# Kernel tuning notes

Hardware: AMD Instinct MI355X
Metric: run time of the kernel (lower is better)

Reference implementation:

```python
import jax, jax.numpy as jnp
import numpy as np

B, CIN, COUT, H, W = 4, 128, 128, 128, 128
K = 3
K2 = K * K
PAD = 1
EPS = 1e-5


def setup_inputs() -> dict:
    key = jax.random.key(0)
    ks = jax.random.split(key, 11)
    def n(k, shp, s=0.05):
        return jax.random.normal(k, shp, jnp.float32) * s
    return {
        'x': jax.random.normal(ks[0], (B, CIN, H, W), jnp.float32),
        'w_attn': n(ks[1], (COUT, CIN, 3, 3)), 'b_attn': n(ks[2], (COUT,)),
        'w_feat': n(ks[3], (COUT, CIN, 3, 3)), 'b_feat': n(ks[4], (COUT,)),
        'w_org': n(ks[5], (COUT, COUT, 3, 3)), 'b_org': n(ks[6], (COUT,)),
        'w_off': n(ks[7], (2 * K2, COUT, 3, 3), 0.01), 'b_off': n(ks[8], (2 * K2,), 0.01),
        'w_mask': n(ks[9], (K2, COUT, 3, 3)), 'b_mask': n(ks[10], (K2,)),
    }


def _conv(x, w, b, stride=1, pad=1):
    y = jax.lax.conv_general_dilated(
        x, w, (stride, stride), [(pad, pad), (pad, pad)],
        dimension_numbers=('NCHW', 'OIHW', 'NCHW'))
    return y + b[None, :, None, None]


def _instance_norm(x):
    mu = jnp.mean(x, axis=(2, 3), keepdims=True)
    var = jnp.var(x, axis=(2, 3), keepdims=True)
    return (x - mu) * jax.lax.rsqrt(var + EPS)


def _lrelu(x):
    return jnp.where(x > 0, x, 0.2 * x)


def _bilinear_gather(img, y, x):
    Hin, Win = img.shape[2], img.shape[3]
    y0 = jnp.floor(y)
    x0 = jnp.floor(x)
    wy = y - y0
    wx = x - x0
    y0i = y0.astype(jnp.int32)
    x0i = x0.astype(jnp.int32)
    acc = None
    for dy, dx, w in ((0, 0, (1 - wy) * (1 - wx)), (0, 1, (1 - wy) * wx),
                      (1, 0, wy * (1 - wx)), (1, 1, wy * wx)):
        yi = y0i + dy
        xi = x0i + dx
        valid = (yi >= 0) & (yi < Hin) & (xi >= 0) & (xi < Win)
        yc = jnp.clip(yi, 0, Hin - 1)
        xc = jnp.clip(xi, 0, Win - 1)
        g = jax.vmap(lambda im, yy, xx: im[:, yy, xx])(img, yc, xc)  # [B,C,K2,H,W]
        ww = (w * valid.astype(img.dtype))[:, None]
        acc = g * ww if acc is None else acc + g * ww
    return acc


def _deform_conv(x, w_org, b_org, w_off, b_off, w_mask, b_mask):
    # torchvision-style modulated deform_conv2d, K=3, stride=1, pad=1
    b, c, h, w = x.shape
    offset = _conv(x, w_off, b_off, 1, 1)                       # [B,2*K2,H,W]
    mask = jax.nn.sigmoid(_conv(x, w_mask, b_mask, 1, 1))       # [B,K2,H,W]
    off = offset.reshape(b, K2, 2, h, w)
    dy, dx = off[:, :, 0], off[:, :, 1]
    ki = jnp.arange(K2, dtype=jnp.float32) // K                 # tap row (row-major)
    kj = jnp.arange(K2, dtype=jnp.float32) % K                  # tap col
    hh = jnp.arange(h, dtype=jnp.float32)
    wwg = jnp.arange(w, dtype=jnp.float32)
    y = dy + hh[None, None, :, None] + ki[None, :, None, None] - PAD
    xs = dx + wwg[None, None, None, :] + kj[None, :, None, None] - PAD
    samp = _bilinear_gather(x, y, xs)                           # [B,C,K2,H,W]
    samp = samp * mask[:, None]
    wflat = w_org.reshape(w_org.shape[0], c, K2)
    out = jnp.einsum('bckhw,ock->bohw', samp, wflat)
    return out + b_org[None, :, None, None]


def reference(x, w_attn, b_attn, w_feat, b_feat, w_org, b_org,
              w_off, b_off, w_mask, b_mask):
    attn = jax.nn.sigmoid(_conv(x, w_attn, b_attn, 1, 1))
    x_feat = _lrelu(_instance_norm(_conv(x, w_feat, b_feat, 1, 1)))
    x_attned = x_feat * attn
    dconv = _deform_conv(x_attned, w_org, b_org, w_off, b_off, w_mask, b_mask)
    x_valid = _lrelu(_instance_norm(dconv))
    return x_attned + x_valid * (1 - attn)
```

## Files before the change

### kernel.cpp

```cpp
#include <hip/hip_runtime.h>
#include <math.h>

#define BDIM 256
constexpr int BB = 4, Cc = 128, Hh = 128, Wd = 128, HW = Hh * Wd;
constexpr float EPSv = 1e-5f;

typedef __attribute__((ext_vector_type(8))) short short8v;
typedef __attribute__((ext_vector_type(4))) float floatx4;
typedef __attribute__((ext_vector_type(2))) float float2v;

#define MFMA16(a, b, c) __builtin_amdgcn_mfma_f32_16x16x32_bf16((a), (b), (c), 0, 0, 0)

__device__ __forceinline__ float sigmoidf_(float v) { return 1.f / (1.f + __expf(-v)); }

__device__ __forceinline__ unsigned short f2bf(float f) {
    union { float f; unsigned u; } v; v.f = f;
    unsigned r = v.u + 0x7FFFu + ((v.u >> 16) & 1u);
    return (unsigned short)(r >> 16);
}
__device__ __forceinline__ unsigned cvtpk(float a, float b) {
    unsigned r;
    asm("v_cvt_pk_bf16_f32 %0, %1, %2" : "=v"(r) : "v"(a), "v"(b));
    return r;
}
__device__ __forceinline__ float bflo(unsigned u) { union { unsigned u; float f; } v; v.u = u << 16; return v.f; }
__device__ __forceinline__ float bfhi(unsigned u) { union { unsigned u; float f; } v; v.u = u & 0xFFFF0000u; return v.f; }
__device__ __forceinline__ float bfu(unsigned short u) { union { unsigned u; float f; } v; v.u = ((unsigned)u) << 16; return v.f; }
__device__ __forceinline__ float2v unpk2(unsigned u) {
    union { unsigned x[2]; float2v f; } v;
    v.x[0] = u << 16;
    v.x[1] = u & 0xFFFF0000u;
    return v.f;
}

__device__ __forceinline__ void barrier_lgkm() {
    asm volatile("s_waitcnt lgkmcnt(0)" ::: "memory");
    __builtin_amdgcn_s_barrier();
}

__device__ __forceinline__ void gload16(const void* g, void* l) {
    __builtin_amdgcn_global_load_lds(
        (const __attribute__((address_space(1))) unsigned int*)g,
        (__attribute__((address_space(3))) unsigned int*)l, 16, 0, 0);
}

__global__ void repack_all_k(const float* __restrict__ w_attn, const float* __restrict__ w_feat,
                             const float* __restrict__ w_org, const float* __restrict__ w_off,
                             const float* __restrict__ w_mask, const float* __restrict__ b_off,
                             const float* __restrict__ b_mask,
                             unsigned short* __restrict__ wpkAF, unsigned short* __restrict__ wpkO,
                             unsigned short* __restrict__ wpkOM, float* __restrict__ bom) {
    int idx = blockIdx.x * BDIM + threadIdx.x;
    const int TOT = 26 * 18432;
    if (idx < TOT) {
        int seg = idx / 18432, rem = idx % 18432;
        int i = rem & 7, lane = (rem >> 3) & 63, tap = (rem >> 9) % 9, chunk = rem / (9 * 512);
        int lco = lane & 15;
        int ci = chunk * 32 + (lane >> 4) * 8 + i;
        float v = 0.f;
        unsigned short* dst;
        int didx;
        if (seg < 16) {
            int cot = seg & 7;
            const float* w = (seg < 8) ? w_attn : w_feat;
            int co = cot * 16 + lco;
            v = w[((size_t)co * Cc + ci) * 9 + tap];
            dst = wpkAF; didx = idx;
        } else if (seg < 24) {
            int co = (seg - 16) * 16 + lco;
            v = w_org[((size_t)co * Cc + ci) * 9 + tap];
            dst = wpkO; didx = idx - 16 * 18432;
        } else {
            int co = (seg - 24) * 16 + lco;
            if (co < 18)      v = w_off[((size_t)co * Cc + ci) * 9 + tap];
            else if (co < 27) v = w_mask[((size_t)(co - 18) * Cc + ci) * 9 + tap];
            dst = wpkOM; didx = idx - 24 * 18432;
        }
        dst[didx] = f2bf(v);
    } else if (idx < TOT + 32) {
        int j = idx - TOT;
        bom[j] = (j < 18) ? b_off[j] : (j < 27 ? b_mask[j - 18] : 0.f);
    }
}

__global__ __launch_bounds__(256) void tobf_k(const float* __restrict__ x,
                                              unsigned short* __restrict__ dst) {
    const int h = blockIdx.x, b = blockIdx.y;
    const int t = threadIdx.x;
    __shared__ unsigned short lt[16][128];
    const int ciq = t >> 4, wg = t & 15;
    const int w = t >> 1, half = t & 1;
    for (int s = 0; s < 8; s++) {
        const float* p = x + ((size_t)(b * 128 + s * 16 + ciq) * HW + h * 128 + wg * 8);
        float4 a = *(const float4*)p;
        float4 c = *(const float4*)(p + 4);
        *(uint4*)&lt[ciq][wg * 8] =
            make_uint4(cvtpk(a.x, a.y), cvtpk(a.z, a.w), cvtpk(c.x, c.y), cvtpk(c.z, c.w));
        __syncthreads();
        unsigned r[4];
#pragma unroll
        for (int k = 0; k < 4; k++) {
            unsigned lo = lt[half * 8 + 2 * k][w];
            unsigned hi = lt[half * 8 + 2 * k + 1][w];
            r[k] = lo | (hi << 16);
        }
        *(uint4*)(dst + ((size_t)b * HW + h * 128 + w) * 128 + s * 16 + half * 8) =
            make_uint4(r[0], r[1], r[2], r[3]);
        __syncthreads();
    }
}

template <int COTPB, int WCO, bool SWZ>
__global__ __launch_bounds__(256, 2) void conv3_k(
    const unsigned short* __restrict__ src, const unsigned short* __restrict__ wpk,
    const float* __restrict__ biasA, const float* __restrict__ biasB,
    int bsplit, int sigsplit,
    float* __restrict__ out, int ldc, int ch0) {
    constexpr int ROWS = 2;
    constexpr int WPX = 4 / WCO;
    constexpr int PXW = 128 / WPX;
    constexpr int PS = PXW / 16;
    constexpr int HB = 128 / ROWS;

    const int t = threadIdx.x;
    const int lane = t & 63, llo = t & 15, lhi = (t >> 4) & 3;
    const int widu = __builtin_amdgcn_readfirstlane(t >> 6);
    const int wr = widu / WPX, wc = widu % WPX;

    int cbi, h0, b;
    if (SWZ) {
        int n = blockIdx.x;
        int xcd = n & 7, j = n >> 3;
        int g = (j >> 2) * 8 + xcd;
        cbi = j & 3;
        h0 = (g % HB) * ROWS;
        b = g / HB;
    } else {
        cbi = 0;
        h0 = ((int)blockIdx.x % HB) * ROWS;
        b = (int)blockIdx.x / HB;
    }
    const int cotbase = cbi * COTPB + wr * 2;

    __shared__ unsigned short xs[2][4][4][128][8];

    floatx4 acc[2][ROWS][PS];
#pragma unroll
    for (int c = 0; c < 2; c++)
#pragma unroll
        for (int row = 0; row < ROWS; row++)
#pragma unroll
            for (int ps = 0; ps < PS; ps++) acc[c][row][ps] = (floatx4){0.f, 0.f, 0.f, 0.f};

    const unsigned short* srcb = src + ((size_t)b * HW + (size_t)(h0 - 1) * 128) * 128;

    auto stage = [&](int chunk, int buf) {
        const unsigned short* sb = srcb + chunk * 32 + widu * 8;
        unsigned short* db = &xs[buf][widu][0][0][0];
#pragma unroll
        for (int i = 0; i < 8; i++) {
            const unsigned short* g = sb + (size_t)(i * 64 + lane) * 128;
            gload16(g, db + i * 512);
        }
    };

    short8v afr[9][2];

    stage(0, 0);
    __syncthreads();

    for (int chunk = 0; chunk < 4; ++chunk) {
        const int buf = chunk & 1;
        if (chunk < 3) stage(chunk + 1, buf ^ 1);
#pragma unroll
        for (int tap = 0; tap < 9; tap++)
#pragma unroll
            for (int c = 0; c < 2; c++)
                afr[tap][c] = *(const short8v*)(wpk +
                    ((((size_t)(cotbase + c) * 4 + chunk) * 9 + tap) * 64 + lane) * 8);
        const int wcb = wc * PXW;
#pragma unroll
        for (int tap = 0; tap < 9; ++tap) {
            const int r = tap / 3, dx = tap % 3;
#pragma unroll
            for (int row = 0; row < ROWS; row++) {
                const int rowr = row + r;
                const int hh = h0 - 1 + rowr;
                if ((unsigned)hh < 128u) {
#pragma unroll
                    for (int ps = 0; ps < PS; ps++) {
                        int colr = wcb + ps * 16 + llo + dx - 1;
                        int colc = min(max(colr, 0), 127);
                        short8v bfv = *(const short8v*)&xs[buf][lhi][rowr][colc][0];
                        if (colr != colc) bfv = (short8v)(short)0;
#pragma unroll
                        for (int c = 0; c < 2; c++)
                            acc[c][row][ps] = MFMA16(afr[tap][c], bfv, acc[c][row][ps]);
                    }
                }
            }
        }
        __syncthreads();
    }

    const int cbase = cbi * (COTPB * 16);
    const float* bp = (cbase < bsplit) ? biasA : biasB;
    const int bshift = (cbase < bsplit) ? 0 : bsplit;
    const bool dosig = cbase < sigsplit;
#pragma unroll
    for (int c = 0; c < 2; c++)
#pragma unroll
        for (int row = 0; row < ROWS; row++)
#pragma unroll
            for (int ps = 0; ps < PS; ps++)
#pragma unroll
                for (int reg = 0; reg < 4; reg++) {
                    int co = cbase + (wr * 2 + c) * 16 + lhi * 4 + reg;
                    int px = wc * PXW + ps * 16 + llo;
                    float v = acc[c][row][ps][reg] + bp[co - bshift];
                    if (dosig) v = sigmoidf_(v);
                    out[((size_t)b * ldc + ch0 + co) * HW + (h0 + row) * Wd + px] = v;
                }
}

__global__ __launch_bounds__(256) void inorm_stats_k(const float* __restrict__ src,
                                                     float* __restrict__ mu, float* __restrict__ rsig,
                                                     int chTot, int ch0) {
    const int bc = blockIdx.x;
    const int b = bc >> 7, c = bc & 127;
    const float4* p = (const float4*)(src + ((size_t)b * chTot + ch0 + c) * HW);
    float s = 0.f, s2 = 0.f;
    for (int i = threadIdx.x; i < HW / 4; i += BDIM) {
        float4 v = p[i];
        s += v.x + v.y + v.z + v.w;
        s2 += v.x * v.x + v.y * v.y + v.z * v.z + v.w * v.w;
    }
    __shared__ float ss[BDIM], sq[BDIM];
    int t = threadIdx.x;
    ss[t] = s; sq[t] = s2;
    __syncthreads();
    for (int off = BDIM / 2; off > 0; off >>= 1) {
        if (t < off) { ss[t] += ss[t + off]; sq[t] += sq[t + off]; }
        __syncthreads();
    }
    if (t == 0) {
        float m = ss[0] / HW;
        float var = sq[0] / HW - m * m;
        mu[bc] = m;
        rsig[bc] = rsqrtf(var + EPSv);
    }
}

__global__ __launch_bounds__(256) void xattned2_k(const float* __restrict__ rawAF,
                                                  const float* __restrict__ mu,
                                                  const float* __restrict__ rsig,
                                                  unsigned short* __restrict__ xabfG) {
    const int seg = blockIdx.x, h = blockIdx.y, b = blockIdx.z;
    const int t = threadIdx.x;
    __shared__ unsigned short la[64][128];
    const int px4 = t & 15, cl = t >> 4;
#pragma unroll
    for (int p = 0; p < 8; p++) {
        int c = p * 16 + cl;
        int plane = b * 128 + c;
        size_t pixo = (size_t)h * Wd + seg * 64 + px4 * 4;
        float4 a = *(const float4*)(rawAF + ((size_t)b * 256 + c) * HW + pixo);
        float4 f = *(const float4*)(rawAF + ((size_t)b * 256 + 128 + c) * HW + pixo);
        float m = mu[plane], rs = rsig[plane];
        float vs[4];
        float v;
        v = (f.x - m) * rs; v = v > 0.f ? v : 0.2f * v; vs[0] = v * a.x;
        v = (f.y - m) * rs; v = v > 0.f ? v : 0.2f * v; vs[1] = v * a.y;
        v = (f.z - m) * rs; v = v > 0.f ? v : 0.2f * v; vs[2] = v * a.z;
        v = (f.w - m) * rs; v = v > 0.f ? v : 0.2f * v; vs[3] = v * a.w;
#pragma unroll
        for (int j = 0; j < 4; j++) la[px4 * 4 + j][c] = f2bf(vs[j]);
    }
    __syncthreads();
    const int px = t >> 2, part = t & 3;
    const uint4* lp = (const uint4*)&la[px][part * 32];
    unsigned short* dp = xabfG + ((size_t)b * HW + h * 128 + seg * 64 + px) * 128 + part * 32;
    uint4 v0 = lp[0], v1 = lp[1], v2 = lp[2], v3 = lp[3];
    *(uint4*)dp = v0;
    *(uint4*)(dp + 8) = v1;
    *(uint4*)(dp + 16) = v2;
    *(uint4*)(dp + 24) = v3;
}

__global__ __launch_bounds__(256, 4) void deform_mfma_k(
    const unsigned short* __restrict__ xabfG, const float* __restrict__ om,
    const unsigned short* __restrict__ wpkO, const float* __restrict__ b_org,
    float* __restrict__ out, int ldc, int ch0) {
    const int seg = blockIdx.x, h = blockIdx.y, b = blockIdx.z;
    const int t = threadIdx.x;
    const int lane = t & 63, llo = t & 15, lhi = (t >> 4) & 3;
    const int wid = t >> 6;
    const int cb = seg * 32;

    __shared__ unsigned short sv[4][9][32][8];
    __shared__ unsigned xt[8 * 6 * 40];

    int prA[2][4];
    float prW[2][4];
    int prT0[2], prOff[2];
    bool prV[2], prOK[2];

    const float* omb = om + (size_t)b * 32 * HW;
#pragma unroll
    for (int u = 0; u < 2; u++) {
        bool valid;
        int pc;
        if (u == 0) { valid = true; pc = t; }
        else { valid = t < 32; pc = 256 + (t & 31); }
        int tap = pc >> 5, pxl = pc & 31;
        int ww = cb + pxl;
        int pix = h * Wd + ww;
        float dy = omb[(size_t)(2 * tap) * HW + pix];
        float dxv = omb[(size_t)(2 * tap + 1) * HW + pix];
        float msk = sigmoidf_(omb[(size_t)(18 + tap) * HW + pix]);
        float yy = dy + (float)(h + tap / 3 - 1);
        float xx = dxv + (float)(ww + tap % 3 - 1);
        float y0f = floorf(yy), x0f = floorf(xx);
        float wy = yy - y0f, wx = xx - x0f;
        int y0 = (int)y0f, x0 = (int)x0f;
#pragma unroll
        for (int c2 = 0; c2 < 4; c2++) {
            int ddy = c2 >> 1, ddx = c2 & 1;
            int yi = y0 + ddy, xi = x0 + ddx;
            bool vc = (yi >= 0) && (yi < Hh) && (xi >= 0) && (xi < Wd);
            int yc = min(max(yi, 0), Hh - 1), xc = min(max(xi, 0), Wd - 1);
            float wt = (ddy ? wy : 1.f - wy) * (ddx ? wx : 1.f - wx);
            prA[u][c2] = yc * Wd + xc;
            prW[u][c2] = vc ? wt * msk : 0.f;
        }
        int ty0 = y0 - (h - 2);
        int tx0 = x0 - (cb - 2);
        prOK[u] = ((unsigned)ty0 <= 4u) && ((unsigned)tx0 <= 38u);
        prT0[u] = ty0 * 40 + tx0;
        prOff[u] = tap * 32 + pxl;
        prV[u] = valid;
    }

    floatx4 acc[2][2];
#pragma unroll
    for (int c = 0; c < 2; c++)
#pragma unroll
        for (int ps = 0; ps < 2; ps++) acc[c][ps] = (floatx4){0.f, 0.f, 0.f, 0.f};

    const unsigned short* xab = xabfG + (size_t)b * HW * 128;
    unsigned short* svf = &sv[0][0][0][0];

    uint4 U[2];

    auto issue_stage = [&](int nc) {
        const int cbase = nc * 16;
#pragma unroll
        for (int it = 0; it < 2; it++) {
            int task = t + it * 256;
            if (task < 480) {
                int col = task % 40;
                int rg = task / 40;
                int row = rg % 6, grp = rg / 6;
                int r = h - 2 + row, cX = cb - 2 + col;
                int rc = min(max(r, 0), Hh - 1), cc = min(max(cX, 0), Wd - 1);
                U[it] = *(const uint4*)(xab + ((size_t)rc * 128 + cc) * 128 + cbase + grp * 8);
            }
        }
    };

    issue_stage(0);

    for (int chunk = 0; chunk < 4; ++chunk) {
#pragma unroll
        for (int half = 0; half < 2; ++half) {
            barrier_lgkm();
#pragma unroll
            for (int it = 0; it < 2; it++) {
                int task = t + it * 256;
                if (task < 480) {
                    int col = task % 40;
                    int rg = task / 40;
                    int row = rg % 6, grp = rg / 6;
                    int cell = row * 40 + col;
                    xt[(grp * 4 + 0) * 240 + cell] = U[it].x;
                    xt[(grp * 4 + 1) * 240 + cell] = U[it].y;
                    xt[(grp * 4 + 2) * 240 + cell] = U[it].z;
                    xt[(grp * 4 + 3) * 240 + cell] = U[it].w;
                }
            }
            int nc = chunk * 2 + half + 1;
            if (nc < 8) issue_stage(nc);
            barrier_lgkm();
#pragma unroll
            for (int u = 0; u < 2; u++) {
                if (!prV[u]) continue;
                const float w0 = prW[u][0], w1 = prW[u][1], w2 = prW[u][2], w3 = prW[u][3];
                if (prOK[u]) {
                    const unsigned* xp = xt + prT0[u];
                    unsigned q[8];
#pragma unroll
                    for (int c2 = 0; c2 < 8; c2++) {
                        unsigned c00 = xp[0], c01 = xp[1];
                        unsigned c10 = xp[40], c11 = xp[41];
                        float2v s = unpk2(c00) * w0 + unpk2(c01) * w1
                                  + unpk2(c10) * w2 + unpk2(c11) * w3;
                        q[c2] = cvtpk(s[0], s[1]);
                        xp += 240;
                    }
                    *(uint4*)(svf + ((size_t)((half * 2 + 0) * 288 + prOff[u]) << 3)) =
                        make_uint4(q[0], q[1], q[2], q[3]);
                    *(uint4*)(svf + ((size_t)((half * 2 + 1) * 288 + prOff[u]) << 3)) =
                        make_uint4(q[4], q[5], q[6], q[7]);
                } else {
                    const int a0 = prA[u][0], a1 = prA[u][1], a2 = prA[u][2], a3 = prA[u][3];
                    const int cch = chunk * 32 + half * 16;
#pragma unroll
                    for (int cg2 = 0; cg2 < 2; cg2++) {
                        unsigned q[4];
#pragma unroll
                        for (int pair = 0; pair < 4; pair++) {
                            int co8 = cch + cg2 * 8 + 2 * pair;
                            unsigned c0 = *(const unsigned*)(xab + (size_t)a0 * 128 + co8);
                            unsigned c1 = *(const unsigned*)(xab + (size_t)a1 * 128 + co8);
                            unsigned c2v = *(const unsigned*)(xab + (size_t)a2 * 128 + co8);
                            unsigned c3 = *(const unsigned*)(xab + (size_t)a3 * 128 + co8);
                            float2v s = unpk2(c0) * w0 + unpk2(c1) * w1
                                      + unpk2(c2v) * w2 + unpk2(c3) * w3;
                            q[pair] = cvtpk(s[0], s[1]);
                        }
                        *(uint4*)(svf + ((size_t)((half * 2 + cg2) * 288 + prOff[u]) << 3)) =
                            make_uint4(q[0], q[1], q[2], q[3]);
                    }
                }
            }
        }
        barrier_lgkm();
#pragma unroll
        for (int tap = 0; tap < 9; ++tap) {
            short8v af[2];
#pragma unroll
            for (int c = 0; c < 2; c++) {
                int cot = wid * 2 + c;
                af[c] = *(const short8v*)(wpkO + ((((size_t)cot * 4 + chunk) * 9 + tap) * 64 + lane) * 8);
            }
            short8v bf[2];
#pragma unroll
            for (int ps = 0; ps < 2; ps++)
                bf[ps] = *(const short8v*)&sv[lhi][tap][ps * 16 + llo][0];
#pragma unroll
            for (int c = 0; c < 2; c++)
#pragma unroll
                for (int ps = 0; ps < 2; ps++)
                    acc[c][ps] = MFMA16(af[c], bf[ps], acc[c][ps]);
        }
    }

#pragma unroll
    for (int c = 0; c < 2; c++)
#pragma unroll
        for (int ps = 0; ps < 2; ps++)
#pragma unroll
            for (int reg = 0; reg < 4; reg++) {
                int co = (wid * 2 + c) * 16 + lhi * 4 + reg;
                int px = cb + ps * 16 + llo;
                out[((size_t)b * ldc + ch0 + co) * HW + h * Wd + px] = acc[c][ps][reg] + b_org[co];
            }
}

__global__ __launch_bounds__(256) void final2_k(const float* __restrict__ rawAF,
                                                const unsigned short* __restrict__ xabfG,
                                                const float* __restrict__ mu,
                                                const float* __restrict__ rsig,
                                                float* __restrict__ outp) {
    const int seg = blockIdx.x, h = blockIdx.y, b = blockIdx.z;
    const int t = threadIdx.x;
    __shared__ unsigned short la[64][128];
    {
        const int px = t >> 2, part = t & 3;
        const unsigned short* sp = xabfG + ((size_t)b * HW + h * 128 + seg * 64 + px) * 128 + part * 32;
        uint4* lp = (uint4*)&la[px][part * 32];
        lp[0] = *(const uint4*)sp;
        lp[1] = *(const uint4*)(sp + 8);
        lp[2] = *(const uint4*)(sp + 16);
        lp[3] = *(const uint4*)(sp + 24);
    }
    __syncthreads();
    const int px4 = t & 15, cl = t >> 4;
#pragma unroll
    for (int p = 0; p < 8; p++) {
        int c = p * 16 + cl;
        int plane = b * 128 + c;
        size_t pixo = (size_t)h * Wd + seg * 64 + px4 * 4;
        float4 a = *(const float4*)(rawAF + ((size_t)b * 256 + c) * HW + pixo);
        float4 d = *(const float4*)(rawAF + ((size_t)b * 256 + 128 + c) * HW + pixo);
        float m = mu[plane], rs = rsig[plane];
        float4 o;
        float v;
        v = (d.x - m) * rs; v = v > 0.f ? v : 0.2f * v; o.x = bfu(la[px4 * 4 + 0][c]) + v * (1.f - a.x);
        v = (d.y - m) * rs; v = v > 0.f ? v : 0.2f * v; o.y = bfu(la[px4 * 4 + 1][c]) + v * (1.f - a.y);
        v = (d.z - m) * rs; v = v > 0.f ? v : 0.2f * v; o.z = bfu(la[px4 * 4 + 2][c]) + v * (1.f - a.z);
        v = (d.w - m) * rs; v = v > 0.f ? v : 0.2f * v; o.w = bfu(la[px4 * 4 + 3][c]) + v * (1.f - a.w);
        *(float4*)(outp + (size_t)plane * HW + pixo) = o;
    }
}

extern "C" void kernel_launch(void* const* d_in, const int* in_sizes, int n_in,
                              void* d_out, int out_size, void* d_ws, size_t ws_size,
                              hipStream_t stream) {
    const float* x      = (const float*)d_in[0];
    const float* w_attn = (const float*)d_in[1];
    const float* b_attn = (const float*)d_in[2];
    const float* w_feat = (const float*)d_in[3];
    const float* b_feat = (const float*)d_in[4];
    const float* w_org  = (const float*)d_in[5];
    const float* b_org  = (const float*)d_in[6];
    const float* w_off  = (const float*)d_in[7];
    const float* b_off  = (const float*)d_in[8];
    const float* w_mask = (const float*)d_in[9];
    const float* b_mask = (const float*)d_in[10];
    float* out = (float*)d_out;
    (void)in_sizes; (void)n_in; (void)out_size; (void)ws_size;

    float* ws = (float*)d_ws;
    float* rawAF = ws;
    unsigned short* regionA = (unsigned short*)(ws + (size_t)BB * 256 * HW);
    unsigned short* xbfG  = regionA + 16384;
    const size_t bfElems = (size_t)BB * HW * 128;
    float* offm = (float*)(regionA + 2 * 16384 + bfElems);
    float* tail = offm + (size_t)BB * 32 * HW;
    unsigned short* wpkAF = (unsigned short*)tail;
    unsigned short* wpkO  = wpkAF + (size_t)16 * 18432;
    unsigned short* wpkOM = wpkO + (size_t)8 * 18432;
    float* bOM = (float*)(wpkOM + (size_t)2 * 18432);
    float* mu1 = bOM + 32;
    float* rs1 = mu1 + 512;
    float* mu2 = rs1 + 512;
    float* rs2 = mu2 + 512;

    repack_all_k<<<(26 * 18432 + 32 + BDIM - 1) / BDIM, BDIM, 0, stream>>>(
        w_attn, w_feat, w_org, w_off, w_mask, b_off, b_mask, wpkAF, wpkO, wpkOM, bOM);

    tobf_k<<<dim3(Hh, BB), BDIM, 0, stream>>>(x, xbfG);

    conv3_k<4, 2, true><<<1024, BDIM, 0, stream>>>(
        xbfG, wpkAF, b_attn, b_feat, 128, 128, rawAF, 256, 0);

    inorm_stats_k<<<BB * Cc, BDIM, 0, stream>>>(rawAF, mu1, rs1, 256, 128);

    xattned2_k<<<dim3(2, Hh, BB), BDIM, 0, stream>>>(rawAF, mu1, rs1, xbfG);

    conv3_k<2, 1, false><<<256, BDIM, 0, stream>>>(
        xbfG, wpkOM, bOM, bOM, 32, 0, offm, 32, 0);

    deform_mfma_k<<<dim3(4, Hh, BB), BDIM, 0, stream>>>(
        xbfG, offm, wpkO, b_org, rawAF, 256, 128);

    inorm_stats_k<<<BB * Cc, BDIM, 0, stream>>>(rawAF, mu2, rs2, 256, 128);

    final2_k<<<dim3(2, Hh, BB), BDIM, 0, stream>>>(rawAF, xbfG, mu2, rs2, out);
}
```

Measured before the change: 206.6 us.

## Fuse instance-norm statistics into conv epilogues via atomics; double-buffer weight fragments

Drops the two separate inorm_stats passes. The feature conv and the deform conv now reduce per-channel sum and sum-of-squares in registers and shuffles, then accumulate them into zeroed global buffers with atomics. Consumers compute mean and rsqrt from those sums. The conv3 weight fragments are also double-buffered so the next chunk's weights load during the current MFMAs. The changes remove two full reads of 64MB-class tensors, at the cost of atomic contention, higher register pressure, and a less numerically stable E[x^2]-m^2 variance.

```diff
diff --git a/kernel.cpp b/kernel.cpp
--- a/kernel.cpp
+++ b/kernel.cpp
@@ -23,8 +23,6 @@
     asm("v_cvt_pk_bf16_f32 %0, %1, %2" : "=v"(r) : "v"(a), "v"(b));
     return r;
 }
-__device__ __forceinline__ float bflo(unsigned u) { union { unsigned u; float f; } v; v.u = u << 16; return v.f; }
-__device__ __forceinline__ float bfhi(unsigned u) { union { unsigned u; float f; } v; v.u = u & 0xFFFF0000u; return v.f; }
 __device__ __forceinline__ float bfu(unsigned short u) { union { unsigned u; float f; } v; v.u = ((unsigned)u) << 16; return v.f; }
 __device__ __forceinline__ float2v unpk2(unsigned u) {
     union { unsigned x[2]; float2v f; } v;
@@ -49,7 +47,8 @@
                              const float* __restrict__ w_mask, const float* __restrict__ b_off,
                              const float* __restrict__ b_mask,
                              unsigned short* __restrict__ wpkAF, unsigned short* __restrict__ wpkO,
-                             unsigned short* __restrict__ wpkOM, float* __restrict__ bom) {
+                             unsigned short* __restrict__ wpkOM, float* __restrict__ bom,
+                             float* __restrict__ statsZ) {
     int idx = blockIdx.x * BDIM + threadIdx.x;
     const int TOT = 26 * 18432;
     if (idx < TOT) {
@@ -80,6 +79,8 @@
     } else if (idx < TOT + 32) {
         int j = idx - TOT;
         bom[j] = (j < 18) ? b_off[j] : (j < 27 ? b_mask[j - 18] : 0.f);
+    } else if (idx < TOT + 32 + 2048) {
+        statsZ[idx - TOT - 32] = 0.f;
     }
 }
 
@@ -110,12 +111,13 @@
     }
 }
 
-template <int COTPB, int WCO, bool SWZ>
+template <int COTPB, int WCO, bool SWZ, bool STATS>
 __global__ __launch_bounds__(256, 2) void conv3_k(
     const unsigned short* __restrict__ src, const unsigned short* __restrict__ wpk,
     const float* __restrict__ biasA, const float* __restrict__ biasB,
     int bsplit, int sigsplit,
-    float* __restrict__ out, int ldc, int ch0) {
+    float* __restrict__ out, int ldc, int ch0,
+    float* __restrict__ S1, float* __restrict__ S2) {
     constexpr int ROWS = 2;
     constexpr int WPX = 4 / WCO;
     constexpr int PXW = 128 / WPX;
@@ -164,21 +166,29 @@
         }
     };
 
-    short8v afr[9][2];
+    short8v afrA[9][2], afrB[9][2];
+    auto loadafr = [&](int chunk, short8v (*dst)[2]) {
+#pragma unroll
+        for (int tap = 0; tap < 9; tap++)
+#pragma unroll
+            for (int c = 0; c < 2; c++)
+                dst[tap][c] = *(const short8v*)(wpk +
+                    ((((size_t)(cotbase + c) * 4 + chunk) * 9 + tap) * 64 + lane) * 8);
+    };
 
     stage(0, 0);
+    loadafr(0, afrA);
     __syncthreads();
 
+    const int wcb = wc * PXW;
+#pragma unroll
     for (int chunk = 0; chunk < 4; ++chunk) {
         const int buf = chunk & 1;
-        if (chunk < 3) stage(chunk + 1, buf ^ 1);
-#pragma unroll
-        for (int tap = 0; tap < 9; tap++)
-#pragma unroll
-            for (int c = 0; c < 2; c++)
-                afr[tap][c] = *(const short8v*)(wpk +
-                    ((((size_t)(cotbase + c) * 4 + chunk) * 9 + tap) * 64 + lane) * 8);
-        const int wcb = wc * PXW;
+        if (chunk < 3) {
+            stage(chunk + 1, buf ^ 1);
+            loadafr(chunk + 1, (chunk & 1) ? afrA : afrB);
+        }
+        short8v (*cur)[2] = (chunk & 1) ? afrB : afrA;
 #pragma unroll
         for (int tap = 0; tap < 9; ++tap) {
             const int r = tap / 3, dx = tap % 3;
@@ -195,7 +205,7 @@
                         if (colr != colc) bfv = (short8v)(short)0;
 #pragma unroll
                         for (int c = 0; c < 2; c++)
-                            acc[c][row][ps] = MFMA16(afr[tap][c], bfv, acc[c][row][ps]);
+                            acc[c][row][ps] = MFMA16(cur[tap][c], bfv, acc[c][row][ps]);
                     }
                 }
             }
@@ -221,39 +231,39 @@
                     if (dosig) v = sigmoidf_(v);
                     out[((size_t)b * ldc + ch0 + co) * HW + (h0 + row) * Wd + px] = v;
                 }
-}
-
-__global__ __launch_bounds__(256) void inorm_stats_k(const float* __restrict__ src,
-                                                     float* __restrict__ mu, float* __restrict__ rsig,
-                                                     int chTot, int ch0) {
-    const int bc = blockIdx.x;
-    const int b = bc >> 7, c = bc & 127;
-    const float4* p = (const float4*)(src + ((size_t)b * chTot + ch0 + c) * HW);
-    float s = 0.f, s2 = 0.f;
-    for (int i = threadIdx.x; i < HW / 4; i += BDIM) {
-        float4 v = p[i];
-        s += v.x + v.y + v.z + v.w;
-        s2 += v.x * v.x + v.y * v.y + v.z * v.z + v.w * v.w;
-    }
-    __shared__ float ss[BDIM], sq[BDIM];
-    int t = threadIdx.x;
-    ss[t] = s; sq[t] = s2;
-    __syncthreads();
-    for (int off = BDIM / 2; off > 0; off >>= 1) {
-        if (t < off) { ss[t] += ss[t + off]; sq[t] += sq[t + off]; }
-        __syncthreads();
-    }
-    if (t == 0) {
-        float m = ss[0] / HW;
-        float var = sq[0] / HW - m * m;
-        mu[bc] = m;
-        rsig[bc] = rsqrtf(var + EPSv);
+
+    if (STATS && cbase >= bsplit) {
+#pragma unroll
+        for (int c = 0; c < 2; c++)
+#pragma unroll
+            for (int reg = 0; reg < 4; reg++) {
+                int co = cbase + (wr * 2 + c) * 16 + lhi * 4 + reg;
+                float bv = bp[co - bshift];
+                float s = 0.f, s2 = 0.f;
+#pragma unroll
+                for (int row = 0; row < ROWS; row++)
+#pragma unroll
+                    for (int ps = 0; ps < PS; ps++) {
+                        float v = acc[c][row][ps][reg] + bv;
+                        s += v; s2 += v * v;
+                    }
+#pragma unroll
+                for (int m = 1; m < 16; m <<= 1) {
+                    s += __shfl_xor(s, m, 64);
+                    s2 += __shfl_xor(s2, m, 64);
+                }
+                if (llo == 0) {
+                    int plane = b * 128 + (co - bsplit);
+                    atomicAdd(&S1[plane], s);
+                    atomicAdd(&S2[plane], s2);
+                }
+            }
     }
 }
 
 __global__ __launch_bounds__(256) void xattned2_k(const float* __restrict__ rawAF,
-                                                  const float* __restrict__ mu,
-                                                  const float* __restrict__ rsig,
+                                                  const float* __restrict__ S1,
+                                                  const float* __restrict__ S2,
                                                   unsigned short* __restrict__ xabfG) {
     const int seg = blockIdx.x, h = blockIdx.y, b = blockIdx.z;
     const int t = threadIdx.x;
@@ -266,7 +276,8 @@
         size_t pixo = (size_t)h * Wd + seg * 64 + px4 * 4;
         float4 a = *(const float4*)(rawAF + ((size_t)b * 256 + c) * HW + pixo);
         float4 f = *(const float4*)(rawAF + ((size_t)b * 256 + 128 + c) * HW + pixo);
-        float m = mu[plane], rs = rsig[plane];
+        float m = S1[plane] * (1.f / HW);
+        float rs = rsqrtf(S2[plane] * (1.f / HW) - m * m + EPSv);
         float vs[4];
         float v;
         v = (f.x - m) * rs; v = v > 0.f ? v : 0.2f * v; vs[0] = v * a.x;
@@ -290,7 +301,8 @@
 __global__ __launch_bounds__(256, 4) void deform_mfma_k(
     const unsigned short* __restrict__ xabfG, const float* __restrict__ om,
     const unsigned short* __restrict__ wpkO, const float* __restrict__ b_org,
-    float* __restrict__ out, int ldc, int ch0) {
+    float* __restrict__ out, int ldc, int ch0,
+    float* __restrict__ S1d, float* __restrict__ S2d) {
     const int seg = blockIdx.x, h = blockIdx.y, b = blockIdx.z;
     const int t = threadIdx.x;
     const int lane = t & 63, llo = t & 15, lhi = (t >> 4) & 3;
@@ -465,12 +477,36 @@
                 int px = cb + ps * 16 + llo;
                 out[((size_t)b * ldc + ch0 + co) * HW + h * Wd + px] = acc[c][ps][reg] + b_org[co];
             }
+
+#pragma unroll
+    for (int c = 0; c < 2; c++)
+#pragma unroll
+        for (int reg = 0; reg < 4; reg++) {
+            int co = (wid * 2 + c) * 16 + lhi * 4 + reg;
+            float bv = b_org[co];
+            float s = 0.f, s2 = 0.f;
+#pragma unroll
+            for (int ps = 0; ps < 2; ps++) {
+                float v = acc[c][ps][reg] + bv;
+                s += v; s2 += v * v;
+            }
+#pragma unroll
+            for (int m = 1; m < 16; m <<= 1) {
+                s += __shfl_xor(s, m, 64);
+                s2 += __shfl_xor(s2, m, 64);
+            }
+            if (llo == 0) {
+                int plane = b * 128 + co;
+                atomicAdd(&S1d[plane], s);
+                atomicAdd(&S2d[plane], s2);
+            }
+        }
 }
 
 __global__ __launch_bounds__(256) void final2_k(const float* __restrict__ rawAF,
                                                 const unsigned short* __restrict__ xabfG,
-                                                const float* __restrict__ mu,
-                                                const float* __restrict__ rsig,
+                                                const float* __restrict__ S1d,
+                                                const float* __restrict__ S2d,
                                                 float* __restrict__ outp) {
     const int seg = blockIdx.x, h = blockIdx.y, b = blockIdx.z;
     const int t = threadIdx.x;
@@ -493,7 +529,8 @@
         size_t pixo = (size_t)h * Wd + seg * 64 + px4 * 4;
         float4 a = *(const float4*)(rawAF + ((size_t)b * 256 + c) * HW + pixo);
         float4 d = *(const float4*)(rawAF + ((size_t)b * 256 + 128 + c) * HW + pixo);
-        float m = mu[plane], rs = rsig[plane];
+        float m = S1d[plane] * (1.f / HW);
+        float rs = rsqrtf(S2d[plane] * (1.f / HW) - m * m + EPSv);
         float4 o;
         float v;
         v = (d.x - m) * rs; v = v > 0.f ? v : 0.2f * v; o.x = bfu(la[px4 * 4 + 0][c]) + v * (1.f - a.x);
@@ -532,30 +569,27 @@
     unsigned short* wpkO  = wpkAF + (size_t)16 * 18432;
     unsigned short* wpkOM = wpkO + (size_t)8 * 18432;
     float* bOM = (float*)(wpkOM + (size_t)2 * 18432);
-    float* mu1 = bOM + 32;
-    float* rs1 = mu1 + 512;
-    float* mu2 = rs1 + 512;
-    float* rs2 = mu2 + 512;
-
-    repack_all_k<<<(26 * 18432 + 32 + BDIM - 1) / BDIM, BDIM, 0, stream>>>(
-        w_attn, w_feat, w_org, w_off, w_mask, b_off, b_mask, wpkAF, wpkO, wpkOM, bOM);
+    float* stats = bOM + 32;
+    float* S1  = stats;
+    float* S2  = stats + 512;
+    float* S1d = stats + 1024;
+    float* S2d = stats + 1536;
+
+    repack_all_k<<<(26 * 18432 + 32 + 2048 + BDIM - 1) / BDIM, BDIM, 0, stream>>>(
+        w_attn, w_feat, w_org, w_off, w_mask, b_off, b_mask, wpkAF, wpkO, wpkOM, bOM, stats);
 
     tobf_k<<<dim3(Hh, BB), BDIM, 0, stream>>>(x, xbfG);
 
-    conv3_k<4, 2, true><<<1024, BDIM, 0, stream>>>(
-        xbfG, wpkAF, b_attn, b_feat, 128, 128, rawAF, 256, 0);
-
-    inorm_stats_k<<<BB * Cc, BDIM, 0, stream>>>(rawAF, mu1, rs1, 256, 128);
-
-    xattned2_k<<<dim3(2, Hh, BB), BDIM, 0, stream>>>(rawAF, mu1, rs1, xbfG);
-
-    conv3_k<2, 1, false><<<256, BDIM, 0, stream>>>(
-        xbfG, wpkOM, bOM, bOM, 32, 0, offm, 32, 0);
+    conv3_k<4, 2, true, true><<<1024, BDIM, 0, stream>>>(
+        xbfG, wpkAF, b_attn, b_feat, 128, 128, rawAF, 256, 0, S1, S2);
+
+    xattned2_k<<<dim3(2, Hh, BB), BDIM, 0, stream>>>(rawAF, S1, S2, xbfG);
+
+    conv3_k<2, 1, false, false><<<256, BDIM, 0, stream>>>(
+        xbfG, wpkOM, bOM, bOM, 32, 0, offm, 32, 0, nullptr, nullptr);
 
     deform_mfma_k<<<dim3(4, Hh, BB), BDIM, 0, stream>>>(
-        xbfG, offm, wpkO, b_org, rawAF, 256, 128);
-
-    inorm_stats_k<<<BB * Cc, BDIM, 0, stream>>>(rawAF, mu2, rs2, 256, 128);
-
-    final2_k<<<dim3(2, Hh, BB), BDIM, 0, stream>>>(rawAF, xbfG, mu2, rs2, out);
-}
+        xbfG, offm, wpkO, b_org, rawAF, 256, 128, S1d, S2d);
+
+    final2_k<<<dim3(2, Hh, BB), BDIM, 0, stream>>>(rawAF, xbfG, S1d, S2d, out);
+}
```

Result: slower. 293.6 us (+42.1%).

## Reorder conv loop by input row and double-buffer weight fragments

Applied to the files above, without the earlier changes.

The implicit-GEMM conv loop now iterates over input rows and column shifts, so each LDS B-fragment is loaded once and reused for every output row and tap that needs it, rather than reloaded per tap and output row. Weight A-fragments for the next chunk are prefetched into a second register set while the current chunk computes, and the chunk loop is fully unrolled. This cuts LDS reads and hides global weight-load latency, at the cost of doubling the registers held for weight fragments, which may lower occupancy or cause spills.

```diff
diff --git a/kernel.cpp b/kernel.cpp
--- a/kernel.cpp
+++ b/kernel.cpp
@@ -23,8 +23,6 @@
     asm("v_cvt_pk_bf16_f32 %0, %1, %2" : "=v"(r) : "v"(a), "v"(b));
     return r;
 }
-__device__ __forceinline__ float bflo(unsigned u) { union { unsigned u; float f; } v; v.u = u << 16; return v.f; }
-__device__ __forceinline__ float bfhi(unsigned u) { union { unsigned u; float f; } v; v.u = u & 0xFFFF0000u; return v.f; }
 __device__ __forceinline__ float bfu(unsigned short u) { union { unsigned u; float f; } v; v.u = ((unsigned)u) << 16; return v.f; }
 __device__ __forceinline__ float2v unpk2(unsigned u) {
     union { unsigned x[2]; float2v f; } v;
@@ -164,29 +162,35 @@
         }
     };
 
-    short8v afr[9][2];
+    short8v afrA[9][2], afrB[9][2];
+    auto loadafr = [&](int chunk, short8v (*dst)[2]) {
+#pragma unroll
+        for (int tap = 0; tap < 9; tap++)
+#pragma unroll
+            for (int c = 0; c < 2; c++)
+                dst[tap][c] = *(const short8v*)(wpk +
+                    ((((size_t)(cotbase + c) * 4 + chunk) * 9 + tap) * 64 + lane) * 8);
+    };
 
     stage(0, 0);
+    loadafr(0, afrA);
     __syncthreads();
 
+    const int wcb = wc * PXW;
+#pragma unroll
     for (int chunk = 0; chunk < 4; ++chunk) {
         const int buf = chunk & 1;
-        if (chunk < 3) stage(chunk + 1, buf ^ 1);
-#pragma unroll
-        for (int tap = 0; tap < 9; tap++)
-#pragma unroll
-            for (int c = 0; c < 2; c++)
-                afr[tap][c] = *(const short8v*)(wpk +
-                    ((((size_t)(cotbase + c) * 4 + chunk) * 9 + tap) * 64 + lane) * 8);
-        const int wcb = wc * PXW;
-#pragma unroll
-        for (int tap = 0; tap < 9; ++tap) {
-            const int r = tap / 3, dx = tap % 3;
-#pragma unroll
-            for (int row = 0; row < ROWS; row++) {
-                const int rowr = row + r;
-                const int hh = h0 - 1 + rowr;
-                if ((unsigned)hh < 128u) {
+        if (chunk < 3) {
+            stage(chunk + 1, buf ^ 1);
+            loadafr(chunk + 1, (chunk & 1) ? afrA : afrB);
+        }
+        short8v (*cur)[2] = (chunk & 1) ? afrB : afrA;
+#pragma unroll
+        for (int rowr = 0; rowr < ROWS + 2; ++rowr) {
+            const int hh = h0 - 1 + rowr;
+            if ((unsigned)hh < 128u) {
+#pragma unroll
+                for (int dx = 0; dx < 3; ++dx) {
 #pragma unroll
                     for (int ps = 0; ps < PS; ps++) {
                         int colr = wcb + ps * 16 + llo + dx - 1;
@@ -194,8 +198,15 @@
                         short8v bfv = *(const short8v*)&xs[buf][lhi][rowr][colc][0];
                         if (colr != colc) bfv = (short8v)(short)0;
 #pragma unroll
-                        for (int c = 0; c < 2; c++)
-                            acc[c][row][ps] = MFMA16(afr[tap][c], bfv, acc[c][row][ps]);
+                        for (int row = 0; row < ROWS; ++row) {
+                            const int r = rowr - row;
+                            if (r >= 0 && r < 3) {
+                                const int tap = r * 3 + dx;
+#pragma unroll
+                                for (int c = 0; c < 2; c++)
+                                    acc[c][row][ps] = MFMA16(cur[tap][c], bfv, acc[c][row][ps]);
+                            }
+                        }
                     }
                 }
             }
```

New measurement: 184.6 us, median of 3. -10.6%, faster.
